# Kernel optimization log

Hardware: AMD Instinct MI355X
Metric: run time of the kernel (lower is better)

## Reference

```python
import jax, jax.numpy as jnp
import numpy as np

T, B, F, L = 512, 4096, 16, 4  # seq_len, batch, input_size, n_layers; hidden_size H = 1


def _lstm_layer(seq, W_ih, W_hh, b_ih, b_hh):
    """Single unidirectional LSTM layer, H=1.
    seq: [T, B, in]; W_ih: [4, in]; W_hh: [4, 1]; b_ih, b_hh: [4].
    Returns (hs [T,B,1], h_T [B,1], c_T [B,1]). Gate order i,f,g,o (PyTorch).
    """
    # Input contribution for all timesteps at once (the only sizeable GEMM).
    gx = jnp.einsum('tbi,gi->tbg', seq, W_ih) + b_ih + b_hh  # [T, B, 4]
    Bb = seq.shape[1]
    h0 = jnp.zeros((Bb, 1), seq.dtype)
    c0 = jnp.zeros((Bb, 1), seq.dtype)

    def step(carry, g):
        h, c = carry
        gates = g + h @ W_hh.T  # [B, 4]
        i = jax.nn.sigmoid(gates[:, 0:1])
        f = jax.nn.sigmoid(gates[:, 1:2])
        gg = jnp.tanh(gates[:, 2:3])
        o = jax.nn.sigmoid(gates[:, 3:4])
        c = f * c + i * gg
        h = o * jnp.tanh(c)
        return (h, c), h

    (hT, cT), hs = jax.lax.scan(step, (h0, c0), gx)
    return hs, hT, cT


def setup_inputs() -> dict:
    key = jax.random.key(0)
    ks = jax.random.split(key, 6)
    s = 0.5  # ~U(-1,1) stdev scale; 1/sqrt(H)=1 in torch init
    return {
        'x': jax.random.normal(ks[0], (T, B, F), jnp.float32),
        'W_ih0': jax.random.normal(ks[1], (4, F), jnp.float32) * s,
        'W_ih_rest': jax.random.normal(ks[2], (L - 1, 4, 1), jnp.float32) * s,
        'W_hh': jax.random.normal(ks[3], (L, 4, 1), jnp.float32) * s,
        'b_ih': jax.random.normal(ks[4], (L, 4), jnp.float32) * s,
        'b_hh': jax.random.normal(ks[5], (L, 4), jnp.float32) * s,
    }


def reference(x, W_ih0, W_ih_rest, W_hh, b_ih, b_hh):
    seq = x
    hns, cns = [], []
    for l in range(L):
        W_ih_l = W_ih0 if l == 0 else W_ih_rest[l - 1]
        seq, hT, cT = _lstm_layer(seq, W_ih_l, W_hh[l], b_ih[l], b_hh[l])
        hns.append(hT)
        cns.append(cT)
    output = seq                      # [T, B, 1] last-layer hidden sequence
    hn = jnp.stack(hns, axis=0)       # [L, B, 1]
    cn = jnp.stack(cns, axis=0)       # [L, B, 1]
    return output, hn, cn
```

## Files before the change

kernel.cpp:

```cpp
#include <hip/hip_runtime.h>

#define T_DIM 512
#define B_DIM 4096
#define L_DIM 4
#define LOG2E 1.44269504088896f

typedef float f4 __attribute__((ext_vector_type(4)));

__device__ __forceinline__ float dpp_prev(float v) {
  int r = __builtin_amdgcn_update_dpp(0, __builtin_bit_cast(int, v),
                                      0x111 , 0xf, 0xf, true);
  return __builtin_bit_cast(float, r);
}
template <int CTRL>
__device__ __forceinline__ float qp_add(float v) {
  int r = __builtin_amdgcn_update_dpp(0, __builtin_bit_cast(int, v),
                                      CTRL, 0xf, 0xf, true);
  return v + __builtin_bit_cast(float, r);
}

__device__ __forceinline__ void ld_f4(f4& dst, unsigned voff, const f4* base) {
  asm volatile("global_load_dwordx4 %0, %1, %2"
               : "=v"(dst) : "v"(voff), "s"(base) : "memory");
}
__device__ __forceinline__ void wait_ring(f4* buf) {
  asm volatile("s_waitcnt vmcnt(0)"
               : "+v"(buf[0]), "+v"(buf[1]), "+v"(buf[2]), "+v"(buf[3]),
                 "+v"(buf[4]), "+v"(buf[5]), "+v"(buf[6]), "+v"(buf[7])
               :: "memory");
}

__global__ __launch_bounds__(64, 1) void lstm_fused(
    const float* __restrict__ x,
    const float* __restrict__ Wih0,
    const float* __restrict__ Wrest,
    const float* __restrict__ Whh,
    const float* __restrict__ bih, const float* __restrict__ bhh,
    float* __restrict__ out) {
  const int lane = threadIdx.x;
  const int l = lane & 3;
  const int b = blockIdx.x * 16 + (lane >> 2);
  const bool l0 = (l == 0);
  const float gsel = l0 ? 1.0f : 0.0f;

  const float sg[4] = {-LOG2E, -LOG2E, 2.0f * LOG2E, -LOG2E};

  float wih[4], whh[4], base[4];
  f4 w4[4];
#pragma unroll
  for (int g = 0; g < 4; ++g) {
    whh[g]  = sg[g] * Whh[l * 4 + g];
    wih[g]  = l0 ? 0.0f : sg[g] * Wrest[(l - 1) * 4 + g];
    base[g] = sg[g] * (bih[l * 4 + g] + bhh[l * 4 + g]);
    f4 wv = ((const f4*)Wih0)[g * 4 + l];
    w4[g].x = sg[g] * wv.x; w4[g].y = sg[g] * wv.y;
    w4[g].z = sg[g] * wv.z; w4[g].w = sg[g] * wv.w;
  }

  float* __restrict__ po = out + b;
  float h = 0.f, c = 0.f;
  float hsv[8];

  const char* xb = (const char*)x + (size_t)blockIdx.x * 1024;
  unsigned vj[8];
#pragma unroll
  for (int j = 0; j < 8; ++j) vj[j] = (unsigned)lane * 16u + (unsigned)j * 262144u;

  f4 A[8], Bq[8];

  auto load8 = [&](f4* buf, int t0) {
    const f4* p = (const f4*)(xb + (size_t)t0 * 262144);
#pragma unroll
    for (int j = 0; j < 8; ++j) ld_f4(buf[j], vj[j], p);
  };

  auto cell = [&](int k, int j, f4 xv, bool guard) {
    float p0 = fmaf(xv.w, w4[0].w, fmaf(xv.z, w4[0].z, fmaf(xv.y, w4[0].y, xv.x * w4[0].x)));
    float p1 = fmaf(xv.w, w4[1].w, fmaf(xv.z, w4[1].z, fmaf(xv.y, w4[1].y, xv.x * w4[1].x)));
    float p2 = fmaf(xv.w, w4[2].w, fmaf(xv.z, w4[2].z, fmaf(xv.y, w4[2].y, xv.x * w4[2].x)));
    float p3 = fmaf(xv.w, w4[3].w, fmaf(xv.z, w4[3].z, fmaf(xv.y, w4[3].y, xv.x * w4[3].x)));
    p0 = qp_add<0x4E>(qp_add<0xB1>(p0));
    p1 = qp_add<0x4E>(qp_add<0xB1>(p1));
    p2 = qp_add<0x4E>(qp_add<0xB1>(p2));
    p3 = qp_add<0x4E>(qp_add<0xB1>(p3));

    float hin = dpp_prev(h);

    float g0 = fmaf(whh[0], h, fmaf(wih[0], hin, fmaf(gsel, p0, base[0])));
    float g1 = fmaf(whh[1], h, fmaf(wih[1], hin, fmaf(gsel, p1, base[1])));
    float g2 = fmaf(whh[2], h, fmaf(wih[2], hin, fmaf(gsel, p2, base[2])));
    float g3 = fmaf(whh[3], h, fmaf(wih[3], hin, fmaf(gsel, p3, base[3])));

    float Ad = 1.0f + __builtin_amdgcn_exp2f(g0);
    float Bd = 1.0f + __builtin_amdgcn_exp2f(g1);
    float Cd = 1.0f + __builtin_amdgcn_exp2f(g2);
    float Dd = 1.0f + __builtin_amdgcn_exp2f(g3);
    float rAB = __builtin_amdgcn_rcpf(Ad * Bd);
    float rCD = __builtin_amdgcn_rcpf(Cd * Dd);
    float i_ = rAB * Bd;
    float f_ = rAB * Ad;
    float tg = fmaf(-2.0f, rCD * Dd, 1.0f);
    float o_ = rCD * Cd;

    float cn  = fmaf(f_, c, i_ * tg);
    float ecn = __builtin_amdgcn_exp2f(2.88539008178f * cn);
    float tcn = fmaf(-2.0f, __builtin_amdgcn_rcpf(1.0f + ecn), 1.0f);
    float hn  = o_ * tcn;

    if (guard) {
      const int t = k - l;
      const bool valid = (unsigned)t < (unsigned)T_DIM;
      c = valid ? cn : c;
      h = valid ? hn : h;
    } else {
      c = cn; h = hn;
    }
    hsv[j] = hn;
  };
  auto cells8 = [&](int k0, f4* buf, bool guard) {
#pragma unroll
    for (int j = 0; j < 8; ++j) cell(k0 + j, j, buf[j], guard);
  };
  auto flush = [&](int k0, int jlo, int jhi) {
    if (l == 3) {
#pragma unroll
      for (int j = 0; j < 8; ++j)
        if (j >= jlo && j <= jhi)
          po[(size_t)(k0 + j - 3) * B_DIM] = hsv[j];
    }
  };

  load8(A, 0);
  wait_ring(A);
  load8(Bq, 8);
  cells8(0, A, true);
  wait_ring(Bq); flush(0, 3, 7);  load8(A, 16);  cells8(8, Bq, false);
  wait_ring(A);  flush(8, 0, 7);  load8(Bq, 24); cells8(16, A, false);
#pragma unroll 1
  for (int n = 3; n < 63; n += 2) {
    wait_ring(Bq); flush(8 * (n - 1), 0, 7); load8(A, 8 * (n + 1));
    cells8(8 * n, Bq, false);
    wait_ring(A);  flush(8 * n, 0, 7);       load8(Bq, 8 * (n + 2));
    cells8(8 * (n + 1), A, false);
  }
  wait_ring(Bq); flush(8 * 62, 0, 7);
  cells8(504, Bq, false);
  flush(504, 0, 7);
  cells8(512, Bq, true);
  flush(512, 0, 2);

  po[(size_t)T_DIM * B_DIM + (size_t)l * B_DIM] = h;
  po[(size_t)T_DIM * B_DIM + (size_t)L_DIM * B_DIM + (size_t)l * B_DIM] = c;
}

extern "C" void kernel_launch(void* const* d_in, const int* in_sizes, int n_in,
                              void* d_out, int out_size, void* d_ws, size_t ws_size,
                              hipStream_t stream) {
  const float* x     = (const float*)d_in[0];
  const float* Wih0  = (const float*)d_in[1];
  const float* Wrest = (const float*)d_in[2];
  const float* Whh   = (const float*)d_in[3];
  const float* bih   = (const float*)d_in[4];
  const float* bhh   = (const float*)d_in[5];
  float* out = (float*)d_out;
  lstm_fused<<<B_DIM / 16, 64, 0, stream>>>(x, Wih0, Wrest, Whh, bih, bhh, out);
}
```

Baseline: 262.0 us.

## Spread LSTM gates across lanes, four batch chains per wave

Remaps the wavefront so each lane handles one gate of one layer for one batch chain, giving 4 chains per 64-lane block instead of 16, and launches 4x more blocks. Each lane now does one exp/rcp per step instead of four, and gate values are exchanged with DPP quad broadcasts plus a ds_bpermute for the layer-0 input projection. This shortens the serial dependency chain per timestep and adds more waves to hide latency. In exchange it adds cross-lane shuffles and an LDS-path permute on the critical path, and each wave covers fewer batch elements.

```diff
diff --git a/kernel.cpp b/kernel.cpp
--- a/kernel.cpp
+++ b/kernel.cpp
@@ -7,17 +7,13 @@
 
 typedef float f4 __attribute__((ext_vector_type(4)));
 
-__device__ __forceinline__ float dpp_prev(float v) {
-  int r = __builtin_amdgcn_update_dpp(0, __builtin_bit_cast(int, v),
-                                      0x111 , 0xf, 0xf, true);
+template <int CTRL>
+__device__ __forceinline__ float dpp_mov(float v) {
+  int r = __builtin_amdgcn_update_dpp(0, __builtin_bit_cast(int, v), CTRL, 0xf, 0xf, true);
   return __builtin_bit_cast(float, r);
 }
 template <int CTRL>
-__device__ __forceinline__ float qp_add(float v) {
-  int r = __builtin_amdgcn_update_dpp(0, __builtin_bit_cast(int, v),
-                                      CTRL, 0xf, 0xf, true);
-  return v + __builtin_bit_cast(float, r);
-}
+__device__ __forceinline__ float qp_add(float v) { return v + dpp_mov<CTRL>(v); }
 
 __device__ __forceinline__ void ld_f4(f4& dst, unsigned voff, const f4* base) {
   asm volatile("global_load_dwordx4 %0, %1, %2"
@@ -38,33 +34,37 @@
     const float* __restrict__ bih, const float* __restrict__ bhh,
     float* __restrict__ out) {
   const int lane = threadIdx.x;
-  const int l = lane & 3;
-  const int b = blockIdx.x * 16 + (lane >> 2);
+  const int g = lane & 3;
+  const int l = (lane >> 2) & 3;
+  const int c = (lane >> 4) & 3;
+  const int chain = blockIdx.x * 4 + c;
   const bool l0 = (l == 0);
-  const float gsel = l0 ? 1.0f : 0.0f;
 
-  const float sg[4] = {-LOG2E, -LOG2E, 2.0f * LOG2E, -LOG2E};
+  const float sgo[4] = {-LOG2E, -LOG2E, 2.0f * LOG2E, -LOG2E};
 
-  float wih[4], whh[4], base[4];
-  f4 w4[4];
-#pragma unroll
-  for (int g = 0; g < 4; ++g) {
-    whh[g]  = sg[g] * Whh[l * 4 + g];
-    wih[g]  = l0 ? 0.0f : sg[g] * Wrest[(l - 1) * 4 + g];
-    base[g] = sg[g] * (bih[l * 4 + g] + bhh[l * 4 + g]);
-    f4 wv = ((const f4*)Wih0)[g * 4 + l];
-    w4[g].x = sg[g] * wv.x; w4[g].y = sg[g] * wv.y;
-    w4[g].z = sg[g] * wv.z; w4[g].w = sg[g] * wv.w;
+  const float whh  = sgo[g] * Whh[l * 4 + g];
+  const float wih  = l0 ? 0.f : sgo[g] * Wrest[(l - 1) * 4 + g];
+  const float base = l0 ? 0.f : sgo[g] * (bih[l * 4 + g] + bhh[l * 4 + g]);
+  f4 wx;
+  {
+    const f4 wv = ((const f4*)Wih0)[l * 4 + g];
+    const float s = sgo[l];
+    wx.x = s * wv.x; wx.y = s * wv.y; wx.z = s * wv.z; wx.w = s * wv.w;
   }
+  const float dinit = (g == 0) ? sgo[l] * (bih[l] + bhh[l]) : 0.f;
+  const float vm = (g == 2) ? -2.f : 1.f;
+  const float va = (g == 2) ? 1.f : 0.f;
+  const int bperm_addr = 4 * ((lane & 0x30) | (g << 2));
 
-  float* __restrict__ po = out + b;
-  float h = 0.f, c = 0.f;
+  float* __restrict__ po = out + chain;
+  float h = 0.f, cs = 0.f;
   float hsv[8];
 
-  const char* xb = (const char*)x + (size_t)blockIdx.x * 1024;
+  const char* xb = (const char*)x + (size_t)blockIdx.x * 256;
   unsigned vj[8];
 #pragma unroll
-  for (int j = 0; j < 8; ++j) vj[j] = (unsigned)lane * 16u + (unsigned)j * 262144u;
+  for (int j = 0; j < 8; ++j)
+    vj[j] = (unsigned)(c * 64 + g * 16) + (unsigned)j * 262144u;
 
   f4 A[8], Bq[8];
 
@@ -75,45 +75,35 @@
   };
 
   auto cell = [&](int k, int j, f4 xv, bool guard) {
-    float p0 = fmaf(xv.w, w4[0].w, fmaf(xv.z, w4[0].z, fmaf(xv.y, w4[0].y, xv.x * w4[0].x)));
-    float p1 = fmaf(xv.w, w4[1].w, fmaf(xv.z, w4[1].z, fmaf(xv.y, w4[1].y, xv.x * w4[1].x)));
-    float p2 = fmaf(xv.w, w4[2].w, fmaf(xv.z, w4[2].z, fmaf(xv.y, w4[2].y, xv.x * w4[2].x)));
-    float p3 = fmaf(xv.w, w4[3].w, fmaf(xv.z, w4[3].z, fmaf(xv.y, w4[3].y, xv.x * w4[3].x)));
-    p0 = qp_add<0x4E>(qp_add<0xB1>(p0));
-    p1 = qp_add<0x4E>(qp_add<0xB1>(p1));
-    p2 = qp_add<0x4E>(qp_add<0xB1>(p2));
-    p3 = qp_add<0x4E>(qp_add<0xB1>(p3));
+    float p = fmaf(xv.x, wx.x, fmaf(xv.y, wx.y, fmaf(xv.z, wx.z, fmaf(xv.w, wx.w, dinit))));
+    p = qp_add<0xB1>(p);
+    p = qp_add<0x4E>(p);
+    float D = __builtin_bit_cast(float,
+        __builtin_amdgcn_ds_bpermute(bperm_addr, __builtin_bit_cast(int, p)));
 
-    float hin = dpp_prev(h);
+    float hin = dpp_mov<0x114>(h);
+    float pb = l0 ? D : base;
+    float gate = fmaf(whh, h, fmaf(wih, hin, pb));
 
-    float g0 = fmaf(whh[0], h, fmaf(wih[0], hin, fmaf(gsel, p0, base[0])));
-    float g1 = fmaf(whh[1], h, fmaf(wih[1], hin, fmaf(gsel, p1, base[1])));
-    float g2 = fmaf(whh[2], h, fmaf(wih[2], hin, fmaf(gsel, p2, base[2])));
-    float g3 = fmaf(whh[3], h, fmaf(wih[3], hin, fmaf(gsel, p3, base[3])));
+    float r = __builtin_amdgcn_rcpf(1.0f + __builtin_amdgcn_exp2f(gate));
+    float v = fmaf(vm, r, va);
 
-    float Ad = 1.0f + __builtin_amdgcn_exp2f(g0);
-    float Bd = 1.0f + __builtin_amdgcn_exp2f(g1);
-    float Cd = 1.0f + __builtin_amdgcn_exp2f(g2);
-    float Dd = 1.0f + __builtin_amdgcn_exp2f(g3);
-    float rAB = __builtin_amdgcn_rcpf(Ad * Bd);
-    float rCD = __builtin_amdgcn_rcpf(Cd * Dd);
-    float i_ = rAB * Bd;
-    float f_ = rAB * Ad;
-    float tg = fmaf(-2.0f, rCD * Dd, 1.0f);
-    float o_ = rCD * Cd;
-
-    float cn  = fmaf(f_, c, i_ * tg);
-    float ecn = __builtin_amdgcn_exp2f(2.88539008178f * cn);
-    float tcn = fmaf(-2.0f, __builtin_amdgcn_rcpf(1.0f + ecn), 1.0f);
-    float hn  = o_ * tcn;
+    float f_ = dpp_mov<0x55>(v);
+    float tg = dpp_mov<0xAA>(v);
+    float o_ = dpp_mov<0xFF>(v);
+    float cn = fmaf(f_, cs, v * tg);
+    float tcn = fmaf(-2.0f,
+        __builtin_amdgcn_rcpf(1.0f + __builtin_amdgcn_exp2f(2.88539008178f * cn)), 1.0f);
+    float hm = o_ * tcn;
+    float hn = dpp_mov<0x00>(hm);
 
     if (guard) {
       const int t = k - l;
       const bool valid = (unsigned)t < (unsigned)T_DIM;
-      c = valid ? cn : c;
-      h = valid ? hn : h;
+      cs = valid ? cn : cs;
+      h  = valid ? hn : h;
     } else {
-      c = cn; h = hn;
+      cs = cn; h = hn;
     }
     hsv[j] = hn;
   };
@@ -122,11 +112,10 @@
     for (int j = 0; j < 8; ++j) cell(k0 + j, j, buf[j], guard);
   };
   auto flush = [&](int k0, int jlo, int jhi) {
-    if (l == 3) {
+    if (l == 3 && g == 0) {
 #pragma unroll
       for (int j = 0; j < 8; ++j)
-        if (j >= jlo && j <= jhi)
-          po[(size_t)(k0 + j - 3) * B_DIM] = hsv[j];
+        if (j >= jlo && j <= jhi) po[(size_t)(k0 + j - 3) * B_DIM] = hsv[j];
     }
   };
 
@@ -149,8 +138,10 @@
   cells8(512, Bq, true);
   flush(512, 0, 2);
 
-  po[(size_t)T_DIM * B_DIM + (size_t)l * B_DIM] = h;
-  po[(size_t)T_DIM * B_DIM + (size_t)L_DIM * B_DIM + (size_t)l * B_DIM] = c;
+  if (g == 0) {
+    po[(size_t)T_DIM * B_DIM + (size_t)l * B_DIM] = h;
+    po[(size_t)T_DIM * B_DIM + (size_t)L_DIM * B_DIM + (size_t)l * B_DIM] = cs;
+  }
 }
 
 extern "C" void kernel_launch(void* const* d_in, const int* in_sizes, int n_in,
@@ -163,5 +154,5 @@
   const float* bih   = (const float*)d_in[4];
   const float* bhh   = (const float*)d_in[5];
   float* out = (float*)d_out;
-  lstm_fused<<<B_DIM / 16, 64, 0, stream>>>(x, Wih0, Wrest, Whh, bih, bhh, out);
+  lstm_fused<<<B_DIM / 4, 64, 0, stream>>>(x, Wih0, Wrest, Whh, bih, bhh, out);
 }
```

Result: faster. 246.3 us (-6.0%).
